# Kernel optimization log

Measured on AMD Instinct MI355X. Metric: run time of the kernel, lower is better.

The kernel has to match this reference:

```python
import jax, jax.numpy as jnp
import numpy as np

B, H, W, C = 2, 48, 96, 128
N = H * W
NH, HD = 8, 32
WIN_R = 1
WLEN = 2 * WIN_R + 2
ATTN_NUM = WLEN * WLEN
FIELD_DIM = 2
D_SELF = C + FIELD_DIM + NH * 2   # 146
E_SELF = D_SELF + 1               # 147 (noc embed)
D_CROSS = C + FIELD_DIM           # 130
ATTN_DIM = NH * HD                # 256
HID = C * 2                       # ConvGLU hidden
SCALE = HD ** -0.5


def init_coords():
    gx, gy = jnp.meshgrid(jnp.arange(W, dtype=jnp.float32), jnp.arange(H, dtype=jnp.float32))
    return jnp.stack([gx, gy], axis=-1)[None]  # [1,H,W,2] (x,y)


def layer_norm(x, g, b, eps=1e-5):
    mu = x.mean(-1, keepdims=True)
    var = ((x - mu) ** 2).mean(-1, keepdims=True)
    return (x - mu) * jax.lax.rsqrt(var + eps) * g + b


def swap_halves(t):
    a, b = jnp.split(t, 2, axis=0)
    return jnp.concatenate([b, a], axis=0)


def bilinear_sample(img, coords):
    # img [B,H,W,C]; coords [B,H,W,2] absolute (x,y)
    x = jnp.clip(coords[..., 0], 0.0, W - 1.0)
    y = jnp.clip(coords[..., 1], 0.0, H - 1.0)
    x0 = jnp.clip(jnp.floor(x), 0, W - 2).astype(jnp.int32); x1 = x0 + 1
    y0 = jnp.clip(jnp.floor(y), 0, H - 2).astype(jnp.int32); y1 = y0 + 1
    wx = (x - x0)[..., None]; wy = (y - y0)[..., None]
    bi = jnp.arange(img.shape[0])[:, None, None]
    v00 = img[bi, y0, x0]; v01 = img[bi, y0, x1]
    v10 = img[bi, y1, x0]; v11 = img[bi, y1, x1]
    return (1 - wy) * ((1 - wx) * v00 + wx * v01) + wy * ((1 - wx) * v10 + wx * v11)


def consistency_mask(field, A=2.0):
    offset = field + init_coords()
    f_t2r = bilinear_sample(swap_halves(field), offset)
    diff = jnp.abs(field + f_t2r).sum(-1, keepdims=True)
    return (diff < A).astype(field.dtype)  # [B,H,W,1]


def match_attention_core(q, k, v, max_offset):
    # q,k,v: [B,N,NH,HD]; max_offset: [B,N,NH,2] absolute (x,y)
    r = WIN_R
    ox = jnp.clip(max_offset[..., 0], float(r), W - 1 - r - 0.001)
    oy = jnp.clip(max_offset[..., 1], float(r), H - 1 - r - 0.001)
    mxf = jnp.floor(ox); myf = jnp.floor(oy)
    fx = (ox - mxf).transpose(0, 2, 1)[..., None, None]  # [B,NH,N,1,1]
    fy = (oy - myf).transpose(0, 2, 1)[..., None, None]
    mx = mxf.astype(jnp.int32).transpose(0, 2, 1)  # [B,NH,N]
    my = myf.astype(jnp.int32).transpose(0, 2, 1)
    qh = q.transpose(0, 2, 1, 3); kh = k.transpose(0, 2, 1, 3); vh = v.transpose(0, 2, 1, 3)
    dxs = jnp.arange(WLEN) - r                    # window: floor-r .. floor+r+1
    gx = mx[..., None] + dxs                      # [B,NH,N,WLEN]
    gy = my[..., None] + dxs
    idx = (gy[..., :, None] * W + gx[..., None, :]).reshape(B, NH, N, ATTN_NUM)
    bi = jnp.arange(B)[:, None, None, None]
    hi = jnp.arange(NH)[None, :, None, None]
    kg = kh[bi, hi, idx]                          # [B,NH,N,ATTN_NUM,HD]
    s = jnp.einsum('bhnd,bhnad->bhna', qh, kg) * SCALE
    S = s.reshape(B, NH, N, WLEN, WLEN)           # [..., y, x]
    w00 = (1 - fy) * (1 - fx); w01 = (1 - fy) * fx; w10 = fy * (1 - fx); w11 = fy * fx
    # continuous (2r+1)^2 window scores by bilinear interp of integer-grid scores
    s_cont = (w00 * S[..., :-1, :-1] + w01 * S[..., :-1, 1:]
              + w10 * S[..., 1:, :-1] + w11 * S[..., 1:, 1:])
    p = jax.nn.softmax(s_cont.reshape(B, NH, N, -1), axis=-1).reshape(s_cont.shape)
    # scatter continuous probs back to the (2r+2)^2 integer grid with bilinear weights
    Ag = jnp.zeros((B, NH, N, WLEN, WLEN), p.dtype)
    Ag = Ag.at[..., :-1, :-1].add(w00 * p)
    Ag = Ag.at[..., :-1, 1:].add(w01 * p)
    Ag = Ag.at[..., 1:, :-1].add(w10 * p)
    Ag = Ag.at[..., 1:, 1:].add(w11 * p)
    Af = Ag.reshape(B, NH, N, ATTN_NUM)
    vg = vh[bi, hi, idx]                          # [B,NH,N,ATTN_NUM,HD]
    out = jnp.einsum('bhna,bhnad->bhnd', Af, vg)
    return out.transpose(0, 2, 1, 3).reshape(B, N, ATTN_DIM), Af.transpose(0, 2, 1, 3)


def reference(x, self_rpos, field, field_scale, n0_g, n0_b, n1_g, n1_b, n2_g, n2_b,
              sq_w, sk_w, sv_w, sp_w, cq_w, ck_w, cv_w, cg_w, cp_w,
              fc1_w, fc1_b, dw_w, dw_b, fc2_w, fc2_b):
    noc = consistency_mask(jax.lax.stop_gradient(field))
    xc = jnp.concatenate([x, field * field_scale, self_rpos], axis=-1)  # [B,H,W,D_SELF]
    coords0 = jnp.tile(init_coords(), (1, 1, 1, NH))  # [1,H,W,2*NH]
    self_off = (self_rpos + coords0).reshape(B, N, NH, 2)
    # --- self MatchAttention (noc_embed) ---
    h0 = layer_norm(xc, n0_g, n0_b).reshape(B, N, D_SELF)
    xe = jnp.concatenate([h0, noc.reshape(B, N, 1)], axis=-1)
    q = (xe @ sq_w).reshape(B, N, NH, HD)
    k = (xe @ sk_w).reshape(B, N, NH, HD)
    v = (xe @ sv_w).reshape(B, N, NH, HD)
    o, _ = match_attention_core(q, k, v, self_off)
    xc = xc + (o @ sp_w).reshape(B, H, W, D_SELF)
    self_rpos_out = xc[..., -NH * 2:]
    xc = xc[..., :D_CROSS]
    xc = xc.at[..., -1].set(0.0)  # stereo: zero y-flow
    field1 = xc[..., -FIELD_DIM:] / field_scale
    off = (jnp.tile(field1, (1, 1, 1, NH)) + coords0).reshape(B, N, NH, 2)
    # --- cross MatchAttention ---
    h1 = layer_norm(xc, n1_g, n1_b).reshape(B, N, D_CROSS)
    ref = h1
    tgt = swap_halves(h1)
    g = jax.nn.silu(ref @ cg_w)
    q = (ref @ cq_w).reshape(B, N, NH, HD)
    k = (tgt @ ck_w).reshape(B, N, NH, HD)
    v = (tgt @ cv_w).reshape(B, N, NH, HD)
    o, attn = match_attention_core(q, k, v, off)
    o = jnp.concatenate([g * o, attn.reshape(B, N, NH * ATTN_NUM)], axis=-1)
    xc = xc + (o @ cp_w).reshape(B, H, W, D_CROSS)
    xc = xc.at[..., -1].set(0.0)
    field2 = xc[..., -FIELD_DIM:] / field_scale
    xo = xc[..., :C]
    # --- ConvGLU MLP ---
    h2 = layer_norm(xo, n2_g, n2_b)
    u = h2 @ fc1_w + fc1_b
    a, gv = jnp.split(u, 2, axis=-1)
    a = jax.lax.conv_general_dilated(a, dw_w, (1, 1), 'SAME',
                                     dimension_numbers=('NHWC', 'HWIO', 'NHWC'),
                                     feature_group_count=HID) + dw_b
    a = jax.nn.gelu(a, approximate=False) * gv
    xo = xo + (a @ fc2_w + fc2_b)
    return xo, self_rpos_out, field2


def setup_inputs() -> dict:
    key = jax.random.key(0)
    ks = jax.random.split(key, 16)
    def rn(i, shape, s=1.0):
        return jax.random.normal(ks[i], shape, dtype=jnp.float32) * s
    return {
        'x': rn(0, (B, H, W, C)),
        'self_rpos': rn(1, (B, H, W, NH * 2)),
        'field': rn(2, (B, H, W, FIELD_DIM)),
        'field_scale': 0.1 * jnp.ones((1, 1, 1, 2), jnp.float32),
        'n0_g': jnp.ones((D_SELF,), jnp.float32), 'n0_b': jnp.zeros((D_SELF,), jnp.float32),
        'n1_g': jnp.ones((D_CROSS,), jnp.float32), 'n1_b': jnp.zeros((D_CROSS,), jnp.float32),
        'n2_g': jnp.ones((C,), jnp.float32), 'n2_b': jnp.zeros((C,), jnp.float32),
        'sq_w': rn(3, (E_SELF, ATTN_DIM), 0.02), 'sk_w': rn(4, (E_SELF, ATTN_DIM), 0.02),
        'sv_w': rn(5, (E_SELF, ATTN_DIM), 0.02), 'sp_w': rn(6, (ATTN_DIM, D_SELF), 0.02),
        'cq_w': rn(7, (D_CROSS, ATTN_DIM), 0.02), 'ck_w': rn(8, (D_CROSS, ATTN_DIM), 0.02),
        'cv_w': rn(9, (D_CROSS, ATTN_DIM), 0.02), 'cg_w': rn(10, (D_CROSS, ATTN_DIM), 0.02),
        'cp_w': rn(11, (ATTN_DIM + NH * ATTN_NUM, D_CROSS), 0.02),
        'fc1_w': rn(12, (C, 2 * HID), 0.02), 'fc1_b': jnp.zeros((2 * HID,), jnp.float32),
        'dw_w': rn(13, (3, 3, 1, HID), 0.1), 'dw_b': jnp.zeros((HID,), jnp.float32),
        'fc2_w': rn(14, (HID, C), 0.02), 'fc2_b': jnp.zeros((C,), jnp.float32),
    }
```

## Files before the change

### kernel.cpp

```cpp
#include <hip/hip_runtime.h>
#include <math.h>

namespace {
constexpr int Bn = 2, Hh = 48, Ww = 96, Cch = 128;
constexpr int Nn = Hh * Ww;
constexpr int NHh = 8;
constexpr int DSELF = 146, ESELF = 147, DCROSS = 130;
constexpr int Mrows = Bn * Nn;
constexpr float SCALEf = 0.17677669529663687f;
}

typedef float f32x4 __attribute__((ext_vector_type(4)));
typedef short s16x8 __attribute__((ext_vector_type(8)));
typedef _Float16 h16x4 __attribute__((ext_vector_type(4)));

__device__ __forceinline__ unsigned short f2b(float f) {
  unsigned int u = __float_as_uint(f);
  u = u + 0x7fffu + ((u >> 16) & 1u);
  return (unsigned short)(u >> 16);
}
__device__ __forceinline__ float b2f(unsigned short u) {
  return __uint_as_float((unsigned int)u << 16);
}
__device__ __forceinline__ float4 ld4h(const _Float16* p) {
  h16x4 h = *reinterpret_cast<const h16x4*>(p);
  return make_float4((float)h[0], (float)h[1], (float)h[2], (float)h[3]);
}

__device__ __forceinline__ f32x4 mfma_bf16(s16x8 a, s16x8 b, f32x4 c) {
  f32x4 d;
  asm volatile("v_mfma_f32_16x16x32_bf16 %0, %1, %2, %3"
               : "=&v"(d) : "v"(a), "v"(b), "v"(c));
  return d;
}

__device__ __forceinline__ float wave_bcast_sum(float v) {
#pragma unroll
  for (int off = 32; off > 0; off >>= 1) v += __shfl_down(v, off);
  return __shfl(v, 0);
}

struct WDesc { const float* src; int K, N, Kp, dstOff, blkOff; };
struct WPack { WDesc d[11]; };

__device__ __forceinline__ void convert_w_body(const WPack& p, unsigned short* dst,
                                               int bi) {
  int mi = 0;
#pragma unroll
  for (int i = 1; i < 11; i++) if (bi >= p.d[i].blkOff) mi = i;
  WDesc w = p.d[mi];
  int e = (bi - w.blkOff) * 2048 + threadIdx.x * 8;
  int total = w.N * w.Kp;
  if (e >= total) return;
  int n = e / w.Kp, k0 = e - n * w.Kp;
  s16x8 pack;
#pragma unroll
  for (int j = 0; j < 8; j++) {
    int kk = k0 + j;
    float vv = (kk < w.K) ? w.src[(size_t)kk * w.N + n] : 0.f;
    pack[j] = (short)f2b(vv);
  }
  *reinterpret_cast<s16x8*>(dst + w.dstOff + e) = pack;
}

__device__ __forceinline__ void gemm_store(
    float vv, int row, int col, int N, int colSplit,
    const float* __restrict__ bias, const float* __restrict__ resid,
    void* __restrict__ out0, void* __restrict__ out1, int mode0, int act) {
  if (bias) vv += bias[col];
  if (act == 1 || (act == 3 && col >= 256 && col < 512))
    vv = vv / (1.f + expf(-vv));
  if (col < colSplit) {
    if (resid) vv += resid[(size_t)row * colSplit + col];
    if (mode0)
      ((unsigned short*)out0)[(size_t)row * colSplit + col] = f2b(vv);
    else
      ((float*)out0)[(size_t)row * colSplit + col] = vv;
  } else {
    ((_Float16*)out1)[(size_t)row * (N - colSplit) + (col - colSplit)] =
        (_Float16)vv;
  }
}

__global__ __launch_bounds__(256) void mfma_gemm_kernel(
    const unsigned short* __restrict__ A, int Kp,
    const unsigned short* __restrict__ Wt, int N,
    const float* __restrict__ bias, const float* __restrict__ resid,
    void* __restrict__ out0, void* __restrict__ out1, int colSplit,
    int mode0, int swapMode, int act) {
  __shared__ unsigned short As[64 * 40];
  __shared__ unsigned short Bs[64 * 40];
  int tid = threadIdx.x;
  int m0 = blockIdx.y * 64, n0 = blockIdx.x * 64;
  int lane = tid & 63, wv = tid >> 6;
  int wr = wv >> 1, wc = wv & 1;
  int lr = lane & 15, lk = (lane >> 4) * 8;
  int sr = tid >> 2, sk8 = (tid & 3) * 8;
  int am = m0 + sr;
  int swp = (swapMode == 1) || (swapMode == 2 && n0 >= colSplit);
  if (swp) am = (am < Mrows / 2) ? am + Mrows / 2 : am - Mrows / 2;
  const unsigned short* aptr = A + (size_t)am * Kp + sk8;
  int bn = n0 + sr;
  const unsigned short* bptr = (bn < N) ? Wt + (size_t)bn * Kp + sk8 : nullptr;
  f32x4 acc00 = {}, acc01 = {}, acc10 = {}, acc11 = {};
  for (int k0 = 0; k0 < Kp; k0 += 32) {
    s16x8 av = *reinterpret_cast<const s16x8*>(aptr + k0);
    s16x8 bv = {};
    if (bptr) bv = *reinterpret_cast<const s16x8*>(bptr + k0);
    *reinterpret_cast<s16x8*>(&As[sr * 40 + sk8]) = av;
    *reinterpret_cast<s16x8*>(&Bs[sr * 40 + sk8]) = bv;
    __syncthreads();
    s16x8 a0 = *reinterpret_cast<const s16x8*>(&As[(wr * 32 + lr) * 40 + lk]);
    s16x8 a1 = *reinterpret_cast<const s16x8*>(&As[(wr * 32 + 16 + lr) * 40 + lk]);
    s16x8 b0 = *reinterpret_cast<const s16x8*>(&Bs[(wc * 32 + lr) * 40 + lk]);
    s16x8 b1 = *reinterpret_cast<const s16x8*>(&Bs[(wc * 32 + 16 + lr) * 40 + lk]);
    acc00 = mfma_bf16(a0, b0, acc00);
    acc01 = mfma_bf16(a0, b1, acc01);
    acc10 = mfma_bf16(a1, b0, acc10);
    acc11 = mfma_bf16(a1, b1, acc11);
    __syncthreads();
  }
  int rowBase = m0 + wr * 32 + (lane >> 4) * 4;
  f32x4 accs[2][2] = {{acc00, acc01}, {acc10, acc11}};
#pragma unroll
  for (int fc = 0; fc < 2; fc++) {
    int col = n0 + wc * 32 + fc * 16 + lr;
    if (col >= N) continue;
#pragma unroll
    for (int fr = 0; fr < 2; fr++) {
#pragma unroll
      for (int r = 0; r < 4; r++) {
        int row = rowBase + fr * 16 + r;
        gemm_store(accs[fr][fc][r], row, col, N, colSplit, bias, resid,
                   out0, out1, mode0, act);
      }
    }
  }
}

__global__ __launch_bounds__(128) void mfma_gemm32_kernel(
    const unsigned short* __restrict__ A, int Kp,
    const unsigned short* __restrict__ Wt, int N,
    const float* __restrict__ bias, const float* __restrict__ resid,
    void* __restrict__ out0, void* __restrict__ out1, int colSplit,
    int mode0, int swapMode, int act) {
  __shared__ unsigned short As[32 * 40];
  __shared__ unsigned short Bs[64 * 40];
  int tid = threadIdx.x;
  int m0 = blockIdx.y * 32, n0 = blockIdx.x * 64;
  int lane = tid & 63, wv = tid >> 6;
  int lr = lane & 15, lk = (lane >> 4) * 8;
  int sr = tid >> 2, sk8 = (tid & 3) * 8;
  int am = m0 + sr;
  int swp = (swapMode == 1) || (swapMode == 2 && n0 >= colSplit);
  if (swp) am = (am < Mrows / 2) ? am + Mrows / 2 : am - Mrows / 2;
  const unsigned short* aptr = A + (size_t)am * Kp + sk8;
  int bn0 = n0 + sr, bn1 = n0 + sr + 32;
  const unsigned short* bptr0 = (bn0 < N) ? Wt + (size_t)bn0 * Kp + sk8 : nullptr;
  const unsigned short* bptr1 = (bn1 < N) ? Wt + (size_t)bn1 * Kp + sk8 : nullptr;
  f32x4 acc00 = {}, acc01 = {}, acc10 = {}, acc11 = {};
  for (int k0 = 0; k0 < Kp; k0 += 32) {
    s16x8 av = *reinterpret_cast<const s16x8*>(aptr + k0);
    s16x8 bv0 = {}, bv1 = {};
    if (bptr0) bv0 = *reinterpret_cast<const s16x8*>(bptr0 + k0);
    if (bptr1) bv1 = *reinterpret_cast<const s16x8*>(bptr1 + k0);
    *reinterpret_cast<s16x8*>(&As[sr * 40 + sk8]) = av;
    *reinterpret_cast<s16x8*>(&Bs[sr * 40 + sk8]) = bv0;
    *reinterpret_cast<s16x8*>(&Bs[(sr + 32) * 40 + sk8]) = bv1;
    __syncthreads();
    s16x8 a0 = *reinterpret_cast<const s16x8*>(&As[lr * 40 + lk]);
    s16x8 a1 = *reinterpret_cast<const s16x8*>(&As[(16 + lr) * 40 + lk]);
    s16x8 b0 = *reinterpret_cast<const s16x8*>(&Bs[(wv * 32 + lr) * 40 + lk]);
    s16x8 b1 = *reinterpret_cast<const s16x8*>(&Bs[(wv * 32 + 16 + lr) * 40 + lk]);
    acc00 = mfma_bf16(a0, b0, acc00);
    acc01 = mfma_bf16(a0, b1, acc01);
    acc10 = mfma_bf16(a1, b0, acc10);
    acc11 = mfma_bf16(a1, b1, acc11);
    __syncthreads();
  }
  int rowBase = m0 + (lane >> 4) * 4;
  f32x4 accs[2][2] = {{acc00, acc01}, {acc10, acc11}};
#pragma unroll
  for (int fc = 0; fc < 2; fc++) {
    int col = n0 + wv * 32 + fc * 16 + lr;
    if (col >= N) continue;
#pragma unroll
    for (int fr = 0; fr < 2; fr++) {
#pragma unroll
      for (int r = 0; r < 4; r++) {
        int row = rowBase + fr * 16 + r;
        gemm_store(accs[fr][fc][r], row, col, N, colSplit, bias, resid,
                   out0, out1, mode0, act);
      }
    }
  }
}

__global__ __launch_bounds__(256) void prep_kernel(
    WPack wp, unsigned short* __restrict__ warena, int nconv,
    const float* __restrict__ x, const float* __restrict__ rpos,
    const float* __restrict__ field, const float* __restrict__ fs,
    const float* __restrict__ n0g, const float* __restrict__ n0b,
    float* __restrict__ xc, unsigned short* __restrict__ xe_b) {
  if (blockIdx.x < (unsigned)nconv) {
    convert_w_body(wp, warena, blockIdx.x);
    return;
  }
  int wv = threadIdx.x >> 6, lane = threadIdx.x & 63;
  int pix = (blockIdx.x - nconv) * 4 + wv;
  int b = pix / Nn, n = pix - b * Nn;
  int py = n / Ww, px = n - py * Ww;
  const float* xrow = x + (size_t)pix * Cch;
  const float* rrow = rpos + (size_t)pix * 16;
  float f0 = field[(size_t)pix * 2 + 0], f1 = field[(size_t)pix * 2 + 1];
  float fsx = fs[0], fsy = fs[1];
  float vals[3];
#pragma unroll
  for (int i = 0; i < 3; i++) {
    int c = lane + i * 64;
    float v = 0.f;
    if (c < Cch) v = xrow[c];
    else if (c == 128) v = f0 * fsx;
    else if (c == 129) v = f1 * fsy;
    else if (c < DSELF) v = rrow[c - 130];
    vals[i] = v;
  }
  float* xcrow = xc + (size_t)pix * DSELF;
#pragma unroll
  for (int i = 0; i < 3; i++) {
    int c = lane + i * 64;
    if (c < DSELF) xcrow[c] = vals[i];
  }
  float s = 0.f;
#pragma unroll
  for (int i = 0; i < 3; i++) { int c = lane + i * 64; if (c < DSELF) s += vals[i]; }
  float mu = wave_bcast_sum(s) * (1.f / DSELF);
  float s2 = 0.f;
#pragma unroll
  for (int i = 0; i < 3; i++) {
    int c = lane + i * 64;
    if (c < DSELF) { float d = vals[i] - mu; s2 += d * d; }
  }
  float var = wave_bcast_sum(s2) * (1.f / DSELF);
  float rs = rsqrtf(var + 1e-5f);
  float noc = 0.f;
  if (lane == 0) {
    float ox = fminf(fmaxf(f0 + (float)px, 0.f), (float)(Ww - 1));
    float oy = fminf(fmaxf(f1 + (float)py, 0.f), (float)(Hh - 1));
    float x0f = fminf(fmaxf(floorf(ox), 0.f), (float)(Ww - 2));
    float y0f = fminf(fmaxf(floorf(oy), 0.f), (float)(Hh - 2));
    int x0 = (int)x0f, y0 = (int)y0f;
    float wx = ox - x0f, wy = oy - y0f;
    const float* fo = field + (size_t)(1 - b) * Nn * 2;
    const float* p00 = fo + ((size_t)y0 * Ww + x0) * 2;
    const float* p10 = fo + ((size_t)(y0 + 1) * Ww + x0) * 2;
    float v0 = (1.f - wy) * ((1.f - wx) * p00[0] + wx * p00[2]) +
               wy * ((1.f - wx) * p10[0] + wx * p10[2]);
    float v1 = (1.f - wy) * ((1.f - wx) * p00[1] + wx * p00[3]) +
               wy * ((1.f - wx) * p10[1] + wx * p10[3]);
    float diff = fabsf(f0 + v0) + fabsf(f1 + v1);
    noc = (diff < 2.f) ? 1.f : 0.f;
  }
  noc = __shfl(noc, 0);
  unsigned short* xerow = xe_b + (size_t)pix * 160;
#pragma unroll
  for (int i = 0; i < 3; i++) {
    int c = lane + i * 64;
    if (c < 160) {
      float v;
      if (c < DSELF) v = (vals[i] - mu) * rs * n0g[c] + n0b[c];
      else if (c == 146) v = noc;
      else v = 0.f;
      xerow[c] = f2b(v);
    }
  }
}

__global__ __launch_bounds__(256) void attn_wave_kernel(
    const float* __restrict__ qbuf, int qstride, int gOff,
    const _Float16* __restrict__ kvbuf,
    const float* __restrict__ rpos, const float* __restrict__ xc2,
    const float* __restrict__ fs, unsigned short* __restrict__ o, int o_stride,
    int mode) {
  int wv = threadIdx.x >> 6, lane = threadIdx.x & 63;
  int bid = blockIdx.x;
  int swz = (bid & 7) * 288 + (bid >> 3);
  int pix = swz * 4 + wv;
  int b = pix / Nn, n = pix - b * Nn;
  int py = n / Ww, px = n - py * Ww;
  int h = lane >> 3, c = lane & 7;
  size_t row = (size_t)pix;
  float ox, oy;
  if (mode == 0) {
    ox = rpos[row * 16 + 2 * h] + (float)px;
    oy = rpos[row * 16 + 2 * h + 1] + (float)py;
  } else {
    ox = xc2[row * DCROSS + 128] / fs[0] + (float)px;
    oy = (float)py;
  }
  ox = fminf(fmaxf(ox, 1.0f), 93.999f);
  oy = fminf(fmaxf(oy, 1.0f), 45.999f);
  float mxf = floorf(ox), myf = floorf(oy);
  float fx = ox - mxf, fy = oy - myf;
  int mx = (int)mxf, my = (int)myf;
  int base = b * Nn;

  float4 qv = *reinterpret_cast<const float4*>(qbuf + row * qstride + lane * 4);
  float s[16];
#pragma unroll
  for (int j = 0; j < 4; j++) {
    int gy = my - 1 + j;
#pragma unroll
    for (int i = 0; i < 4; i++) {
      int gx = mx - 1 + i;
      int idx = gy * Ww + gx;
      float4 kv = ld4h(kvbuf + (size_t)(base + idx) * 512 + lane * 4);
      float d = qv.x * kv.x + qv.y * kv.y + qv.z * kv.z + qv.w * kv.w;
      d += __shfl_xor(d, 1);
      d += __shfl_xor(d, 2);
      d += __shfl_xor(d, 4);
      s[j * 4 + i] = d * SCALEf;
    }
  }
  float w00 = (1.f - fy) * (1.f - fx), w01 = (1.f - fy) * fx;
  float w10 = fy * (1.f - fx), w11 = fy * fx;
  float sc[9];
#pragma unroll
  for (int j = 0; j < 3; j++)
#pragma unroll
    for (int i = 0; i < 3; i++)
      sc[j * 3 + i] = w00 * s[j * 4 + i] + w01 * s[j * 4 + i + 1] +
                      w10 * s[(j + 1) * 4 + i] + w11 * s[(j + 1) * 4 + i + 1];
  float mval = sc[0];
#pragma unroll
  for (int i = 1; i < 9; i++) mval = fmaxf(mval, sc[i]);
  float p[9], psum = 0.f;
#pragma unroll
  for (int i = 0; i < 9; i++) { p[i] = expf(sc[i] - mval); psum += p[i]; }
  float inv = 1.f / psum;
#pragma unroll
  for (int i = 0; i < 9; i++) p[i] *= inv;
  float Ag[16] = {};
#pragma unroll
  for (int j = 0; j < 3; j++)
#pragma unroll
    for (int i = 0; i < 3; i++) {
      float pv = p[j * 3 + i];
      Ag[j * 4 + i] += w00 * pv;
      Ag[j * 4 + i + 1] += w01 * pv;
      Ag[(j + 1) * 4 + i] += w10 * pv;
      Ag[(j + 1) * 4 + i + 1] += w11 * pv;
    }
  float4 acc = make_float4(0.f, 0.f, 0.f, 0.f);
#pragma unroll
  for (int j = 0; j < 4; j++) {
    int gy = my - 1 + j;
#pragma unroll
    for (int i = 0; i < 4; i++) {
      int gx = mx - 1 + i;
      int idx = gy * Ww + gx;
      float4 vv = ld4h(kvbuf + (size_t)(base + idx) * 512 + 256 + lane * 4);
      float w = Ag[j * 4 + i];
      acc.x += w * vv.x; acc.y += w * vv.y; acc.z += w * vv.z; acc.w += w * vv.w;
    }
  }
  if (gOff >= 0) {
    float4 gg = *reinterpret_cast<const float4*>(qbuf + row * qstride + gOff + lane * 4);
    acc.x *= gg.x; acc.y *= gg.y; acc.z *= gg.z; acc.w *= gg.w;
  }
  unsigned int p0 = (unsigned int)f2b(acc.x) | ((unsigned int)f2b(acc.y) << 16);
  unsigned int p1 = (unsigned int)f2b(acc.z) | ((unsigned int)f2b(acc.w) << 16);
  *reinterpret_cast<uint2*>(o + row * o_stride + lane * 4) = make_uint2(p0, p1);
  if (mode == 1) {
    float a0 = 0.f, a1 = 0.f;
#pragma unroll
    for (int a = 0; a < 8; a++) {
      if (c == a) { a0 = Ag[2 * a]; a1 = Ag[2 * a + 1]; }
    }
    unsigned int pa = (unsigned int)f2b(a0) | ((unsigned int)f2b(a1) << 16);
    *reinterpret_cast<unsigned int*>(o + row * o_stride + 256 + h * 16 + 2 * c) = pa;
  }
}

__global__ __launch_bounds__(256) void post_self_kernel(
    const float* __restrict__ xcn, const float* __restrict__ n1g,
    const float* __restrict__ n1b, float* __restrict__ out_rpos,
    float* __restrict__ xc2, unsigned short* __restrict__ h1_b) {
  int wv = threadIdx.x >> 6, lane = threadIdx.x & 63;
  int pix = blockIdx.x * 4 + wv;
  const float* row = xcn + (size_t)pix * DSELF;
  float vals[3];
#pragma unroll
  for (int i = 0; i < 3; i++) {
    int c = lane + i * 64;
    vals[i] = (c < DSELF) ? row[c] : 0.f;
  }
#pragma unroll
  for (int i = 0; i < 3; i++) {
    int c = lane + i * 64;
    if (c >= 130 && c < 146) out_rpos[(size_t)pix * 16 + (c - 130)] = vals[i];
  }
#pragma unroll
  for (int i = 0; i < 3; i++) {
    int c = lane + i * 64;
    if (c == 129) vals[i] = 0.f;
  }
  float* x2row = xc2 + (size_t)pix * DCROSS;
#pragma unroll
  for (int i = 0; i < 3; i++) {
    int c = lane + i * 64;
    if (c < DCROSS) x2row[c] = vals[i];
  }
  float s = 0.f;
#pragma unroll
  for (int i = 0; i < 3; i++) { int c = lane + i * 64; if (c < DCROSS) s += vals[i]; }
  float mu = wave_bcast_sum(s) * (1.f / DCROSS);
  float s2 = 0.f;
#pragma unroll
  for (int i = 0; i < 3; i++) {
    int c = lane + i * 64;
    if (c < DCROSS) { float d = vals[i] - mu; s2 += d * d; }
  }
  float var = wave_bcast_sum(s2) * (1.f / DCROSS);
  float rs = rsqrtf(var + 1e-5f);
  unsigned short* h1row = h1_b + (size_t)pix * 160;
#pragma unroll
  for (int i = 0; i < 3; i++) {
    int c = lane + i * 64;
    if (c < 160) {
      float v = (c < DCROSS) ? (vals[i] - mu) * rs * n1g[c] + n1b[c] : 0.f;
      h1row[c] = f2b(v);
    }
  }
}

__global__ __launch_bounds__(256) void post_cross_kernel(
    const float* __restrict__ xc2n, const float* __restrict__ fs,
    const float* __restrict__ n2g, const float* __restrict__ n2b,
    float* __restrict__ out_f2, float* __restrict__ xob,
    unsigned short* __restrict__ h2_b) {
  int wv = threadIdx.x >> 6, lane = threadIdx.x & 63;
  int pix = blockIdx.x * 4 + wv;
  const float* row = xc2n + (size_t)pix * DCROSS;
  float vals[3];
#pragma unroll
  for (int i = 0; i < 3; i++) {
    int c = lane + i * 64;
    vals[i] = (c < DCROSS) ? row[c] : 0.f;
  }
  if (lane == 0) out_f2[(size_t)pix * 2 + 0] = vals[2] / fs[0];
  if (lane == 1) out_f2[(size_t)pix * 2 + 1] = 0.f;
  float* xrow = xob + (size_t)pix * Cch;
#pragma unroll
  for (int i = 0; i < 2; i++) {
    int c = lane + i * 64;
    xrow[c] = vals[i];
  }
  float s = vals[0] + vals[1];
  float mu = wave_bcast_sum(s) * (1.f / Cch);
  float d0 = vals[0] - mu, d1 = vals[1] - mu;
  float var = wave_bcast_sum(d0 * d0 + d1 * d1) * (1.f / Cch);
  float rs = rsqrtf(var + 1e-5f);
  unsigned short* h2row = h2_b + (size_t)pix * Cch;
#pragma unroll
  for (int i = 0; i < 2; i++) {
    int c = lane + i * 64;
    h2row[c] = f2b((vals[i] - mu) * rs * n2g[c] + n2b[c]);
  }
}

__global__ __launch_bounds__(256) void dwconv_kernel(
    const unsigned short* __restrict__ ub, const float* __restrict__ dww,
    const float* __restrict__ dwb, unsigned short* __restrict__ aout) {
  int t = blockIdx.x * 256 + threadIdx.x;
  int c8 = (t & 31) * 8;
  int pix = t >> 5;
  int b = pix / Nn, n = pix - b * Nn;
  int py = n / Ww, px = n - py * Ww;
  float acc[8];
#pragma unroll
  for (int j = 0; j < 8; j++) acc[j] = dwb[c8 + j];
#pragma unroll
  for (int ky = 0; ky < 3; ky++) {
    int yy = py + ky - 1;
    if (yy < 0 || yy >= Hh) continue;
#pragma unroll
    for (int kx = 0; kx < 3; kx++) {
      int xx = px + kx - 1;
      if (xx < 0 || xx >= Ww) continue;
      s16x8 uv = *reinterpret_cast<const s16x8*>(
          ub + ((size_t)(b * Nn + yy * Ww + xx)) * 512 + c8);
      const float* wrow = dww + (ky * 3 + kx) * 256 + c8;
#pragma unroll
      for (int j = 0; j < 8; j++)
        acc[j] += b2f((unsigned short)uv[j]) * wrow[j];
    }
  }
  s16x8 gate = *reinterpret_cast<const s16x8*>(ub + (size_t)pix * 512 + 256 + c8);
  s16x8 outp;
#pragma unroll
  for (int j = 0; j < 8; j++) {
    float a = acc[j];
    float ge = 0.5f * a * (1.f + erff(a * 0.70710678118654752f));
    outp[j] = (short)f2b(ge * b2f((unsigned short)gate[j]));
  }
  *reinterpret_cast<s16x8*>(aout + (size_t)pix * 256 + c8) = outp;
}

extern "C" void kernel_launch(void* const* d_in, const int* in_sizes, int n_in,
                              void* d_out, int out_size, void* d_ws, size_t ws_size,
                              hipStream_t stream) {
  (void)in_sizes; (void)n_in; (void)out_size; (void)ws_size;
  const float* x    = (const float*)d_in[0];
  const float* rpos = (const float*)d_in[1];
  const float* field= (const float*)d_in[2];
  const float* fs   = (const float*)d_in[3];
  const float* n0g  = (const float*)d_in[4];
  const float* n0b  = (const float*)d_in[5];
  const float* n1g  = (const float*)d_in[6];
  const float* n1b  = (const float*)d_in[7];
  const float* n2g  = (const float*)d_in[8];
  const float* n2b  = (const float*)d_in[9];
  const float* sq_w = (const float*)d_in[10];
  const float* sk_w = (const float*)d_in[11];
  const float* sv_w = (const float*)d_in[12];
  const float* sp_w = (const float*)d_in[13];
  const float* cq_w = (const float*)d_in[14];
  const float* ck_w = (const float*)d_in[15];
  const float* cv_w = (const float*)d_in[16];
  const float* cg_w = (const float*)d_in[17];
  const float* cp_w = (const float*)d_in[18];
  const float* fc1w = (const float*)d_in[19];
  const float* fc1b = (const float*)d_in[20];
  const float* dww  = (const float*)d_in[21];
  const float* dwb  = (const float*)d_in[22];
  const float* fc2w = (const float*)d_in[23];
  const float* fc2b = (const float*)d_in[24];

  float* ws = (float*)d_ws;
  float* xc    = ws + 0;
  float* xcn   = ws + 1345536;
  float* xc2   = ws + 2691072;
  float* xc2n  = ws + 3889152;
  float* xob   = ws + 5087232;
  unsigned short* xe_b = (unsigned short*)(ws + 6266880);
  unsigned short* h1_b = (unsigned short*)(ws + 7004160);
  unsigned short* h2_b = (unsigned short*)(ws + 7741440);
  float* q32   = ws + 8331264;
  _Float16* kv16 = (_Float16*)(ws + 10690560);
  float* qg    = ws + 13049856;
  unsigned short* o_b    = (unsigned short*)(ws + 17768448);
  unsigned short* ocat_b = (unsigned short*)(ws + 18948096);
  unsigned short* warena = (unsigned short*)(ws + 20717568);
  unsigned short* u_b    = (unsigned short*)qg;
  unsigned short* aconv_b = o_b;

  float* out_xo   = (float*)d_out;
  float* out_rpos = out_xo + 1179648;
  float* out_f2   = out_xo + 1327104;

  const int oSQKV = 0;
  const int oSP   = 122880;
  const int oCQGKV= 160256;
  const int oCP   = 324096;
  const int oF1   = 374016;
  const int oF2   = 439552;
  WPack wp;
  auto setw = [&](int i, const float* src, int K, int N, int Kp, int off) {
    wp.d[i].src = src; wp.d[i].K = K; wp.d[i].N = N; wp.d[i].Kp = Kp;
    wp.d[i].dstOff = off;
  };
  setw(0, sq_w, 147, 256, 160, oSQKV);
  setw(1, sk_w, 147, 256, 160, oSQKV + 40960);
  setw(2, sv_w, 147, 256, 160, oSQKV + 81920);
  setw(3, sp_w, 256, 146, 256, oSP);
  setw(4, cq_w, 130, 256, 160, oCQGKV);
  setw(5, cg_w, 130, 256, 160, oCQGKV + 40960);
  setw(6, ck_w, 130, 256, 160, oCQGKV + 81920);
  setw(7, cv_w, 130, 256, 160, oCQGKV + 122880);
  setw(8, cp_w, 384, 130, 384, oCP);
  setw(9, fc1w, 128, 512, 128, oF1);
  setw(10, fc2w, 256, 128, 256, oF2);
  int nblk = 0;
  for (int i = 0; i < 11; i++) {
    wp.d[i].blkOff = nblk;
    nblk += (wp.d[i].N * wp.d[i].Kp + 2047) / 2048;
  }

  dim3 blk(256);
  auto gemm = [&](const unsigned short* A, int Kp, int woff, int N,
                  const float* bias, const float* resid, void* out0, void* out1,
                  int colSplit, int mode0, int swapMode, int act) {
    if (N <= 384) {
      dim3 grid((N + 63) / 64, Mrows / 32);
      mfma_gemm32_kernel<<<grid, dim3(128), 0, stream>>>(
          A, Kp, warena + woff, N, bias, resid, out0, out1, colSplit, mode0,
          swapMode, act);
    } else {
      dim3 grid((N + 63) / 64, Mrows / 64);
      mfma_gemm_kernel<<<grid, blk, 0, stream>>>(
          A, Kp, warena + woff, N, bias, resid, out0, out1, colSplit, mode0,
          swapMode, act);
    }
  };

  prep_kernel<<<nblk + 2304, blk, 0, stream>>>(wp, warena, nblk, x, rpos, field,
                                               fs, n0g, n0b, xc, xe_b);
  gemm(xe_b, 160, oSQKV, 768, nullptr, nullptr, q32, kv16, 256, 0, 0, 0);
  attn_wave_kernel<<<2304, blk, 0, stream>>>(q32, 256, -1, kv16, rpos, nullptr,
                                             fs, o_b, 256, 0);
  gemm(o_b, 256, oSP, 146, nullptr, xc, xcn, nullptr, 146, 0, 0, 0);
  post_self_kernel<<<2304, blk, 0, stream>>>(xcn, n1g, n1b, out_rpos, xc2, h1_b);
  gemm(h1_b, 160, oCQGKV, 1024, nullptr, nullptr, qg, kv16, 512, 0, 2, 3);
  attn_wave_kernel<<<2304, blk, 0, stream>>>(qg, 512, 256, kv16, nullptr, xc2,
                                             fs, ocat_b, 384, 1);
  gemm(ocat_b, 384, oCP, 130, nullptr, xc2, xc2n, nullptr, 130, 0, 0, 0);
  post_cross_kernel<<<2304, blk, 0, stream>>>(xc2n, fs, n2g, n2b, out_f2, xob, h2_b);
  gemm(h2_b, 128, oF1, 512, fc1b, nullptr, u_b, nullptr, 512, 1, 0, 0);
  dwconv_kernel<<<1152, blk, 0, stream>>>(u_b, dww, dwb, aconv_b);
  gemm(aconv_b, 256, oF2, 128, fc2b, xob, out_xo, nullptr, 128, 0, 0, 0);
}
```

Before: 147.6 us.

## Fuse post-GEMM splits into epilogues and store Q/gate projections in fp16

```diff
diff --git a/kernel.cpp b/kernel.cpp
--- a/kernel.cpp
+++ b/kernel.cpp
@@ -65,13 +65,32 @@
 
 __device__ __forceinline__ void gemm_store(
     float vv, int row, int col, int N, int colSplit,
-    const float* __restrict__ bias, const float* __restrict__ resid,
-    void* __restrict__ out0, void* __restrict__ out1, int mode0, int act) {
+    const float* __restrict__ bias, const float* __restrict__ resid, int rstride,
+    void* __restrict__ out0, void* __restrict__ out1, int mode0, int act,
+    int post, float* __restrict__ aux, const float* __restrict__ fs) {
   if (bias) vv += bias[col];
   if (act == 1 || (act == 3 && col >= 256 && col < 512))
     vv = vv / (1.f + expf(-vv));
+  if (post == 1) {
+    vv += resid[(size_t)row * 146 + col];
+    if (col < 130)
+      ((float*)out0)[(size_t)row * 130 + col] = (col == 129) ? 0.f : vv;
+    else
+      aux[(size_t)row * 16 + (col - 130)] = vv;
+    return;
+  }
+  if (post == 2) {
+    vv += resid[(size_t)row * 130 + col];
+    if (col < 128)
+      ((float*)out0)[(size_t)row * 128 + col] = vv;
+    else if (col == 128)
+      aux[(size_t)row * 2 + 0] = vv / fs[0];
+    else
+      aux[(size_t)row * 2 + 1] = 0.f;
+    return;
+  }
   if (col < colSplit) {
-    if (resid) vv += resid[(size_t)row * colSplit + col];
+    if (resid) vv += resid[(size_t)row * rstride + col];
     if (mode0)
       ((unsigned short*)out0)[(size_t)row * colSplit + col] = f2b(vv);
     else
@@ -85,9 +104,10 @@
 __global__ __launch_bounds__(256) void mfma_gemm_kernel(
     const unsigned short* __restrict__ A, int Kp,
     const unsigned short* __restrict__ Wt, int N,
-    const float* __restrict__ bias, const float* __restrict__ resid,
+    const float* __restrict__ bias, const float* __restrict__ resid, int rstride,
     void* __restrict__ out0, void* __restrict__ out1, int colSplit,
-    int mode0, int swapMode, int act) {
+    int mode0, int swapMode, int swapCol, int act, int post,
+    float* __restrict__ aux, const float* __restrict__ fs) {
   __shared__ unsigned short As[64 * 40];
   __shared__ unsigned short Bs[64 * 40];
   int tid = threadIdx.x;
@@ -97,7 +117,7 @@
   int lr = lane & 15, lk = (lane >> 4) * 8;
   int sr = tid >> 2, sk8 = (tid & 3) * 8;
   int am = m0 + sr;
-  int swp = (swapMode == 1) || (swapMode == 2 && n0 >= colSplit);
+  int swp = (swapMode == 1) || (swapMode == 2 && n0 >= swapCol);
   if (swp) am = (am < Mrows / 2) ? am + Mrows / 2 : am - Mrows / 2;
   const unsigned short* aptr = A + (size_t)am * Kp + sk8;
   int bn = n0 + sr;
@@ -131,8 +151,8 @@
 #pragma unroll
       for (int r = 0; r < 4; r++) {
         int row = rowBase + fr * 16 + r;
-        gemm_store(accs[fr][fc][r], row, col, N, colSplit, bias, resid,
-                   out0, out1, mode0, act);
+        gemm_store(accs[fr][fc][r], row, col, N, colSplit, bias, resid, rstride,
+                   out0, out1, mode0, act, post, aux, fs);
       }
     }
   }
@@ -141,9 +161,10 @@
 __global__ __launch_bounds__(128) void mfma_gemm32_kernel(
     const unsigned short* __restrict__ A, int Kp,
     const unsigned short* __restrict__ Wt, int N,
-    const float* __restrict__ bias, const float* __restrict__ resid,
+    const float* __restrict__ bias, const float* __restrict__ resid, int rstride,
     void* __restrict__ out0, void* __restrict__ out1, int colSplit,
-    int mode0, int swapMode, int act) {
+    int mode0, int swapMode, int swapCol, int act, int post,
+    float* __restrict__ aux, const float* __restrict__ fs) {
   __shared__ unsigned short As[32 * 40];
   __shared__ unsigned short Bs[64 * 40];
   int tid = threadIdx.x;
@@ -152,7 +173,7 @@
   int lr = lane & 15, lk = (lane >> 4) * 8;
   int sr = tid >> 2, sk8 = (tid & 3) * 8;
   int am = m0 + sr;
-  int swp = (swapMode == 1) || (swapMode == 2 && n0 >= colSplit);
+  int swp = (swapMode == 1) || (swapMode == 2 && n0 >= swapCol);
   if (swp) am = (am < Mrows / 2) ? am + Mrows / 2 : am - Mrows / 2;
   const unsigned short* aptr = A + (size_t)am * Kp + sk8;
   int bn0 = n0 + sr, bn1 = n0 + sr + 32;
@@ -189,8 +210,8 @@
 #pragma unroll
       for (int r = 0; r < 4; r++) {
         int row = rowBase + fr * 16 + r;
-        gemm_store(accs[fr][fc][r], row, col, N, colSplit, bias, resid,
-                   out0, out1, mode0, act);
+        gemm_store(accs[fr][fc][r], row, col, N, colSplit, bias, resid, rstride,
+                   out0, out1, mode0, act, post, aux, fs);
       }
     }
   }
@@ -277,8 +298,8 @@
 }
 
 __global__ __launch_bounds__(256) void attn_wave_kernel(
-    const float* __restrict__ qbuf, int qstride, int gOff,
-    const _Float16* __restrict__ kvbuf,
+    const _Float16* __restrict__ qbuf, int qstride, int gOff,
+    const _Float16* __restrict__ kvbuf, int kvstride,
     const float* __restrict__ rpos, const float* __restrict__ xc2,
     const float* __restrict__ fs, unsigned short* __restrict__ o, int o_stride,
     int mode) {
@@ -305,7 +326,7 @@
   int mx = (int)mxf, my = (int)myf;
   int base = b * Nn;
 
-  float4 qv = *reinterpret_cast<const float4*>(qbuf + row * qstride + lane * 4);
+  float4 qv = ld4h(qbuf + row * qstride + lane * 4);
   float s[16];
 #pragma unroll
   for (int j = 0; j < 4; j++) {
@@ -314,7 +335,7 @@
     for (int i = 0; i < 4; i++) {
       int gx = mx - 1 + i;
       int idx = gy * Ww + gx;
-      float4 kv = ld4h(kvbuf + (size_t)(base + idx) * 512 + lane * 4);
+      float4 kv = ld4h(kvbuf + (size_t)(base + idx) * kvstride + lane * 4);
       float d = qv.x * kv.x + qv.y * kv.y + qv.z * kv.z + qv.w * kv.w;
       d += __shfl_xor(d, 1);
       d += __shfl_xor(d, 2);
@@ -359,13 +380,13 @@
     for (int i = 0; i < 4; i++) {
       int gx = mx - 1 + i;
       int idx = gy * Ww + gx;
-      float4 vv = ld4h(kvbuf + (size_t)(base + idx) * 512 + 256 + lane * 4);
+      float4 vv = ld4h(kvbuf + (size_t)(base + idx) * kvstride + 256 + lane * 4);
       float w = Ag[j * 4 + i];
       acc.x += w * vv.x; acc.y += w * vv.y; acc.z += w * vv.z; acc.w += w * vv.w;
     }
   }
   if (gOff >= 0) {
-    float4 gg = *reinterpret_cast<const float4*>(qbuf + row * qstride + gOff + lane * 4);
+    float4 gg = ld4h(qbuf + row * qstride + gOff + lane * 4);
     acc.x *= gg.x; acc.y *= gg.y; acc.z *= gg.z; acc.w *= gg.w;
   }
   unsigned int p0 = (unsigned int)f2b(acc.x) | ((unsigned int)f2b(acc.y) << 16);
@@ -383,33 +404,16 @@
 }
 
 __global__ __launch_bounds__(256) void post_self_kernel(
-    const float* __restrict__ xcn, const float* __restrict__ n1g,
-    const float* __restrict__ n1b, float* __restrict__ out_rpos,
-    float* __restrict__ xc2, unsigned short* __restrict__ h1_b) {
+    const float* __restrict__ xc2, const float* __restrict__ n1g,
+    const float* __restrict__ n1b, unsigned short* __restrict__ h1_b) {
   int wv = threadIdx.x >> 6, lane = threadIdx.x & 63;
   int pix = blockIdx.x * 4 + wv;
-  const float* row = xcn + (size_t)pix * DSELF;
+  const float* row = xc2 + (size_t)pix * DCROSS;
   float vals[3];
 #pragma unroll
   for (int i = 0; i < 3; i++) {
     int c = lane + i * 64;
-    vals[i] = (c < DSELF) ? row[c] : 0.f;
-  }
-#pragma unroll
-  for (int i = 0; i < 3; i++) {
-    int c = lane + i * 64;
-    if (c >= 130 && c < 146) out_rpos[(size_t)pix * 16 + (c - 130)] = vals[i];
-  }
-#pragma unroll
-  for (int i = 0; i < 3; i++) {
-    int c = lane + i * 64;
-    if (c == 129) vals[i] = 0.f;
-  }
-  float* x2row = xc2 + (size_t)pix * DCROSS;
-#pragma unroll
-  for (int i = 0; i < 3; i++) {
-    int c = lane + i * 64;
-    if (c < DCROSS) x2row[c] = vals[i];
+    vals[i] = (c < DCROSS) ? row[c] : 0.f;
   }
   float s = 0.f;
 #pragma unroll
@@ -435,38 +439,19 @@
 }
 
 __global__ __launch_bounds__(256) void post_cross_kernel(
-    const float* __restrict__ xc2n, const float* __restrict__ fs,
-    const float* __restrict__ n2g, const float* __restrict__ n2b,
-    float* __restrict__ out_f2, float* __restrict__ xob,
-    unsigned short* __restrict__ h2_b) {
+    const float* __restrict__ xob, const float* __restrict__ n2g,
+    const float* __restrict__ n2b, unsigned short* __restrict__ h2_b) {
   int wv = threadIdx.x >> 6, lane = threadIdx.x & 63;
   int pix = blockIdx.x * 4 + wv;
-  const float* row = xc2n + (size_t)pix * DCROSS;
-  float vals[3];
-#pragma unroll
-  for (int i = 0; i < 3; i++) {
-    int c = lane + i * 64;
-    vals[i] = (c < DCROSS) ? row[c] : 0.f;
-  }
-  if (lane == 0) out_f2[(size_t)pix * 2 + 0] = vals[2] / fs[0];
-  if (lane == 1) out_f2[(size_t)pix * 2 + 1] = 0.f;
-  float* xrow = xob + (size_t)pix * Cch;
-#pragma unroll
-  for (int i = 0; i < 2; i++) {
-    int c = lane + i * 64;
-    xrow[c] = vals[i];
-  }
-  float s = vals[0] + vals[1];
-  float mu = wave_bcast_sum(s) * (1.f / Cch);
-  float d0 = vals[0] - mu, d1 = vals[1] - mu;
+  const float* row = xob + (size_t)pix * Cch;
+  float v0 = row[lane], v1 = row[lane + 64];
+  float mu = wave_bcast_sum(v0 + v1) * (1.f / Cch);
+  float d0 = v0 - mu, d1 = v1 - mu;
   float var = wave_bcast_sum(d0 * d0 + d1 * d1) * (1.f / Cch);
   float rs = rsqrtf(var + 1e-5f);
   unsigned short* h2row = h2_b + (size_t)pix * Cch;
-#pragma unroll
-  for (int i = 0; i < 2; i++) {
-    int c = lane + i * 64;
-    h2row[c] = f2b((vals[i] - mu) * rs * n2g[c] + n2b[c]);
-  }
+  h2row[lane] = f2b(d0 * rs * n2g[lane] + n2b[lane]);
+  h2row[lane + 64] = f2b(d1 * rs * n2g[lane + 64] + n2b[lane + 64]);
 }
 
 __global__ __launch_bounds__(256) void dwconv_kernel(
@@ -539,20 +524,17 @@
 
   float* ws = (float*)d_ws;
   float* xc    = ws + 0;
-  float* xcn   = ws + 1345536;
-  float* xc2   = ws + 2691072;
-  float* xc2n  = ws + 3889152;
-  float* xob   = ws + 5087232;
-  unsigned short* xe_b = (unsigned short*)(ws + 6266880);
-  unsigned short* h1_b = (unsigned short*)(ws + 7004160);
-  unsigned short* h2_b = (unsigned short*)(ws + 7741440);
-  float* q32   = ws + 8331264;
-  _Float16* kv16 = (_Float16*)(ws + 10690560);
-  float* qg    = ws + 13049856;
-  unsigned short* o_b    = (unsigned short*)(ws + 17768448);
-  unsigned short* ocat_b = (unsigned short*)(ws + 18948096);
-  unsigned short* warena = (unsigned short*)(ws + 20717568);
-  unsigned short* u_b    = (unsigned short*)qg;
+  float* xc2   = ws + 1345536;
+  float* xob   = ws + 2543616;
+  unsigned short* xe_b   = (unsigned short*)(ws + 3723264);
+  unsigned short* h1_b   = (unsigned short*)(ws + 4460544);
+  unsigned short* h2_b   = (unsigned short*)(ws + 5197824);
+  _Float16* qkv16  = (_Float16*)(ws + 5787648);
+  _Float16* qgkv16 = (_Float16*)(ws + 9326592);
+  unsigned short* o_b    = (unsigned short*)(ws + 14045184);
+  unsigned short* ocat_b = (unsigned short*)(ws + 15224832);
+  unsigned short* warena = (unsigned short*)(ws + 16994304);
+  unsigned short* u_b    = (unsigned short*)qkv16;
   unsigned short* aconv_b = o_b;
 
   float* out_xo   = (float*)d_out;
@@ -589,34 +571,42 @@
 
   dim3 blk(256);
   auto gemm = [&](const unsigned short* A, int Kp, int woff, int N,
-                  const float* bias, const float* resid, void* out0, void* out1,
-                  int colSplit, int mode0, int swapMode, int act) {
+                  const float* bias, const float* resid, int rstride,
+                  void* out0, void* out1, int colSplit, int mode0,
+                  int swapMode, int swapCol, int act, int post, float* aux) {
     if (N <= 384) {
       dim3 grid((N + 63) / 64, Mrows / 32);
       mfma_gemm32_kernel<<<grid, dim3(128), 0, stream>>>(
-          A, Kp, warena + woff, N, bias, resid, out0, out1, colSplit, mode0,
-          swapMode, act);
+          A, Kp, warena + woff, N, bias, resid, rstride, out0, out1, colSplit,
+          mode0, swapMode, swapCol, act, post, aux, fs);
     } else {
       dim3 grid((N + 63) / 64, Mrows / 64);
       mfma_gemm_kernel<<<grid, blk, 0, stream>>>(
-          A, Kp, warena + woff, N, bias, resid, out0, out1, colSplit, mode0,
-          swapMode, act);
+          A, Kp, warena + woff, N, bias, resid, rstride, out0, out1, colSplit,
+          mode0, swapMode, swapCol, act, post, aux, fs);
     }
   };
 
   prep_kernel<<<nblk + 2304, blk, 0, stream>>>(wp, warena, nblk, x, rpos, field,
                                                fs, n0g, n0b, xc, xe_b);
-  gemm(xe_b, 160, oSQKV, 768, nullptr, nullptr, q32, kv16, 256, 0, 0, 0);
-  attn_wave_kernel<<<2304, blk, 0, stream>>>(q32, 256, -1, kv16, rpos, nullptr,
-                                             fs, o_b, 256, 0);
-  gemm(o_b, 256, oSP, 146, nullptr, xc, xcn, nullptr, 146, 0, 0, 0);
-  post_self_kernel<<<2304, blk, 0, stream>>>(xcn, n1g, n1b, out_rpos, xc2, h1_b);
-  gemm(h1_b, 160, oCQGKV, 1024, nullptr, nullptr, qg, kv16, 512, 0, 2, 3);
-  attn_wave_kernel<<<2304, blk, 0, stream>>>(qg, 512, 256, kv16, nullptr, xc2,
-                                             fs, ocat_b, 384, 1);
-  gemm(ocat_b, 384, oCP, 130, nullptr, xc2, xc2n, nullptr, 130, 0, 0, 0);
-  post_cross_kernel<<<2304, blk, 0, stream>>>(xc2n, fs, n2g, n2b, out_f2, xob, h2_b);
-  gemm(h2_b, 128, oF1, 512, fc1b, nullptr, u_b, nullptr, 512, 1, 0, 0);
+  gemm(xe_b, 160, oSQKV, 768, nullptr, nullptr, 0, nullptr, qkv16, 0, 0, 0, 0,
+       0, 0, nullptr);
+  attn_wave_kernel<<<2304, blk, 0, stream>>>(qkv16, 768, -1, qkv16 + 256, 768,
+                                             rpos, nullptr, fs, o_b, 256, 0);
+  gemm(o_b, 256, oSP, 146, nullptr, xc, 146, xc2, nullptr, 130, 0, 0, 0, 0, 1,
+       out_rpos);
+  post_self_kernel<<<2304, blk, 0, stream>>>(xc2, n1g, n1b, h1_b);
+  gemm(h1_b, 160, oCQGKV, 1024, nullptr, nullptr, 0, nullptr, qgkv16, 0, 0, 2,
+       512, 3, 0, nullptr);
+  attn_wave_kernel<<<2304, blk, 0, stream>>>(qgkv16, 1024, 256, qgkv16 + 512,
+                                             1024, nullptr, xc2, fs, ocat_b,
+                                             384, 1);
+  gemm(ocat_b, 384, oCP, 130, nullptr, xc2, 130, xob, nullptr, 128, 0, 0, 0, 0,
+       2, out_f2);
+  post_cross_kernel<<<2304, blk, 0, stream>>>(xob, n2g, n2b, h2_b);
+  gemm(h2_b, 128, oF1, 512, fc1b, nullptr, 512, u_b, nullptr, 512, 1, 0, 0, 0,
+       0, nullptr);
   dwconv_kernel<<<1152, blk, 0, stream>>>(u_b, dww, dwb, aconv_b);
-  gemm(aconv_b, 256, oF2, 128, fc2b, xob, out_xo, nullptr, 128, 0, 0, 0);
-}
+  gemm(aconv_b, 256, oF2, 128, fc2b, xob, 128, out_xo, nullptr, 128, 0, 0, 0,
+       0, 0, nullptr);
+}
```

Result: no change. 148.0 us, median of 2 (+0.2%).
